# Optimization experiments

Measured on AMD Instinct MI355X. Metric: run time of the kernel, lower is better.

The kernel has to match this reference:

```python
import jax, jax.numpy as jnp
import numpy as np

N_QUBITS = 10
SAMPLE_LENGTH = 2 ** N_QUBITS  # AmplitudeEmbedding requires len(features) == 2**n
NUM_CLASSES = 10
BATCH = 8192
TOTAL_PARAMS = N_QUBITS + 12 * (N_QUBITS // 2) * 2 + N_QUBITS * 3  # 160
C64 = jnp.complex64

H_GATE = (jnp.array([[1, 1], [1, -1]], dtype=C64) * np.float32(1.0 / np.sqrt(2.0)))
CNOT = jnp.array([[1, 0, 0, 0], [0, 1, 0, 0], [0, 0, 0, 1], [0, 0, 1, 0]], dtype=C64)
CZ = jnp.diag(jnp.array([1, 1, 1, -1], dtype=C64))


def rx(t):
    c = jnp.cos(t / 2).astype(C64)
    s = jnp.sin(t / 2).astype(C64)
    return jnp.stack([jnp.stack([c, -1j * s]), jnp.stack([-1j * s, c])])


def ry(t):
    c = jnp.cos(t / 2).astype(C64)
    s = jnp.sin(t / 2).astype(C64)
    return jnp.stack([jnp.stack([c, -s]), jnp.stack([s, c])])


def rz(t):
    e = jnp.exp(-0.5j * t).astype(C64)
    z = jnp.zeros_like(e)
    return jnp.stack([jnp.stack([e, z]), jnp.stack([z, jnp.conj(e)])])


def rot(phi, theta, omega):
    # qml.Rot = RZ(omega) @ RY(theta) @ RZ(phi)
    return rz(omega) @ ry(theta) @ rz(phi)


def apply_gate(psi, U, wires):
    # psi: (B, 2, 2, ..., 2); U: (2**k, 2**k); wires in PennyLane order (wire 0 = MSB = axis 1)
    k = len(wires)
    U = U.reshape((2,) * (2 * k))
    axes = [1 + w for w in wires]
    psi = jnp.tensordot(U, psi, axes=(list(range(k, 2 * k)), axes))
    return jnp.moveaxis(psi, list(range(k)), axes)


def vqc_block(psi, p, i):
    psi = apply_gate(psi, rx(p[0]), [i])
    psi = apply_gate(psi, ry(p[1]), [i + 1])
    psi = apply_gate(psi, ry(p[2]), [i])
    psi = apply_gate(psi, rz(p[3]), [i + 1])
    psi = apply_gate(psi, rz(p[4]), [i])
    psi = apply_gate(psi, rx(p[5]), [i + 1])
    psi = apply_gate(psi, CZ, [i, i + 1])
    psi = apply_gate(psi, rz(p[6]), [i])
    psi = apply_gate(psi, rx(p[7]), [i + 1])
    psi = apply_gate(psi, ry(p[8]), [i])
    psi = apply_gate(psi, rz(p[9]), [i + 1])
    psi = apply_gate(psi, rx(p[10]), [i])
    psi = apply_gate(psi, ry(p[11]), [i + 1])
    psi = apply_gate(psi, CNOT, [i + 1, i])
    return psi


def circuit(x, all_params):
    n = N_QUBITS
    B = x.shape[0]
    # AmplitudeEmbedding with normalize=True
    norm = jnp.linalg.norm(x, axis=1, keepdims=True)
    psi = (x / norm).astype(C64).reshape((B,) + (2,) * n)
    emb = all_params[:n]
    v1 = all_params[n:n + 12 * (n // 2)].reshape(n // 2, 12)
    v2 = all_params[n + 12 * (n // 2):n + 24 * (n // 2)].reshape(n // 2, 12)
    sel = all_params[n + 24 * (n // 2):].reshape(n, 3)
    # embedding layer: H then RY on each wire
    for i in range(n):
        psi = apply_gate(psi, H_GATE, [i])
    for i in range(n):
        psi = apply_gate(psi, ry(emb[i]), [i])
    # two stacks of VQC blocks on even wire pairs
    for i in range(n // 2):
        psi = vqc_block(psi, v1[i], 2 * i)
    for i in range(n // 2):
        psi = vqc_block(psi, v2[i], 2 * i)
    # CNOT ring
    for i in range(n):
        psi = apply_gate(psi, CNOT, [i, (i + 1) % n])
    # StronglyEntanglingLayers, 1 layer: Rot on each wire, then CNOT ring (range=1)
    for i in range(n):
        psi = apply_gate(psi, rot(sel[i, 0], sel[i, 1], sel[i, 2]), [i])
    for i in range(n):
        psi = apply_gate(psi, CNOT, [i, (i + 1) % n])
    # <Z_i> = sum_s |psi_s|^2 * (1 - 2*bit_i(s)), wire 0 = MSB
    probs = (jnp.abs(psi) ** 2).reshape(B, 2 ** n)
    bits = (jnp.arange(2 ** n)[None, :] >> (n - 1 - jnp.arange(n))[:, None]) & 1
    signs = (1 - 2 * bits).astype(jnp.float32)  # (n, 2**n)
    return probs @ signs.T  # (B, n)


def setup_inputs() -> dict:
    key = jax.random.key(0)
    ks = jax.random.split(key, 4)
    x = jax.random.normal(ks[0], (BATCH, SAMPLE_LENGTH), dtype=jnp.float32)
    all_params = jax.random.normal(ks[1], (TOTAL_PARAMS,), dtype=jnp.float32)
    w_in = jax.random.normal(ks[2], (N_QUBITS, SAMPLE_LENGTH), dtype=jnp.float32) * np.float32(1.0 / np.sqrt(SAMPLE_LENGTH))
    b_in = jnp.zeros((N_QUBITS,), dtype=jnp.float32)
    w_fc = jax.random.normal(ks[3], (NUM_CLASSES, N_QUBITS), dtype=jnp.float32) * np.float32(1.0 / np.sqrt(N_QUBITS))
    b_fc = jnp.zeros((NUM_CLASSES,), dtype=jnp.float32)
    return {"x": x, "all_params": all_params, "w_in": w_in, "b_in": b_in, "w_fc": w_fc, "b_fc": b_fc}


def reference(x, all_params, w_in, b_in, w_fc, b_fc):
    x_proj = x @ w_in.T + b_in          # (B, n_qubits)
    q_out = circuit(x, all_params)      # (B, n_qubits)
    q_out = q_out + x_proj              # residual add (dropout is identity at eval)
    return q_out @ w_fc.T + b_fc        # (B, num_classes)
```

## Files before the change

kernel.cpp:

```cpp
#include <hip/hip_runtime.h>

typedef __attribute__((ext_vector_type(2))) float f2;

#define WAIT_LDS asm volatile("s_waitcnt lgkmcnt(0)" ::: "memory")

__device__ __forceinline__ f2 mk(float a, float b){ f2 r; r.x=a; r.y=b; return r; }

template<int CTRL>
__device__ __forceinline__ float dpp_add(float v){
  int t = __builtin_amdgcn_update_dpp(0, __builtin_bit_cast(int, v), CTRL, 0xF, 0xF, true);
  return v + __builtin_bit_cast(float, t);
}
__device__ __forceinline__ float wave_red_bcast(float v){
  v = dpp_add<0x111>(v);
  v = dpp_add<0x112>(v);
  v = dpp_add<0x114>(v);
  v = dpp_add<0x118>(v);
  v = dpp_add<0x142>(v);
  v = dpp_add<0x143>(v);
  return __builtin_bit_cast(float, __builtin_amdgcn_readlane(__builtin_bit_cast(int, v), 63));
}
template<int CTRL>
__device__ __forceinline__ float dpp_qp(float v){
  int t = __builtin_amdgcn_update_dpp(0, __builtin_bit_cast(int, v), CTRL, 0xF, 0xF, true);
  return __builtin_bit_cast(float, t);
}
#define XT(V,o) ((o)==1 ? dpp_qp<0xB1>(V) : (o)==2 ? dpp_qp<0x4E>(V) : __shfl_xor((V),(o)))

__device__ __forceinline__ void cmadS(f2& c, f2 g, f2 b){
  asm("v_pk_fma_f32 %0, %1, %2, %0 op_sel:[0,0,0] op_sel_hi:[0,1,1]\n\t"
      "v_pk_fma_f32 %0, %1, %2, %0 op_sel:[1,1,0] op_sel_hi:[1,0,1] neg_lo:[1,0,0]"
      : "+v"(c) : "s"(g), "v"(b));
}
__device__ __forceinline__ f2 cmulS(f2 g, f2 b){
  f2 d;
  asm("v_pk_mul_f32 %0, %1, %2 op_sel:[0,0] op_sel_hi:[0,1]\n\t"
      "v_pk_fma_f32 %0, %1, %2, %0 op_sel:[1,1,0] op_sel_hi:[1,0,1] neg_lo:[1,0,0]"
      : "=&v"(d) : "s"(g), "v"(b));
  return d;
}
__device__ __forceinline__ void quadS(const f2* __restrict__ G, f2& a0, f2& a1, f2& a2, f2& a3){
  f2 c0,c1,c2,c3;
  c0=cmulS(G[0],a0);  c1=cmulS(G[1],a0);  c2=cmulS(G[2],a0);  c3=cmulS(G[3],a0);
  cmadS(c0,G[4],a1);  cmadS(c1,G[5],a1);  cmadS(c2,G[6],a1);  cmadS(c3,G[7],a1);
  cmadS(c0,G[8],a2);  cmadS(c1,G[9],a2);  cmadS(c2,G[10],a2); cmadS(c3,G[11],a2);
  cmadS(c0,G[12],a3); cmadS(c1,G[13],a3); cmadS(c2,G[14],a3); cmadS(c3,G[15],a3);
  a0=c0; a1=c1; a2=c2; a3=c3;
}

__device__ __forceinline__ float2 cmul(float2 a, float2 b){
  return make_float2(a.x*b.x - a.y*b.y, a.x*b.y + a.y*b.x);
}
__device__ __forceinline__ float2 cmad(float2 acc, float2 a, float2 b){
  acc.x += a.x*b.x - a.y*b.y; acc.y += a.x*b.y + a.y*b.x; return acc;
}

__global__ __launch_bounds__(64) void qm_setup(
    const float* __restrict__ params, const float* __restrict__ w_fc,
    const float* __restrict__ b_in, const float* __restrict__ b_fc,
    float* __restrict__ wsf){
  __shared__ float2 m2[50][4];
  __shared__ float2 h4[10][16];
  const int t = threadIdx.x;

  if (t < 50){
    int typ[5], pix[5], ng;
    if (t < 40){
      int i = t>>3, k = t&7;
      int P1 = 10 + i*12, P2 = 70 + i*12;
      switch(k){
        case 0: ng=5; typ[0]=3;pix[0]=0;     typ[1]=1;pix[1]=2*i;   typ[2]=0;pix[2]=P1+0;
                      typ[3]=1;pix[3]=P1+2;  typ[4]=2;pix[4]=P1+4;  break;
        case 1: ng=5; typ[0]=3;pix[0]=0;     typ[1]=1;pix[1]=2*i+1; typ[2]=1;pix[2]=P1+1;
                      typ[3]=2;pix[3]=P1+3;  typ[4]=0;pix[4]=P1+5;  break;
        case 2: ng=3; typ[0]=2;pix[0]=P1+6;  typ[1]=1;pix[1]=P1+8;  typ[2]=0;pix[2]=P1+10; break;
        case 3: ng=3; typ[0]=0;pix[0]=P1+7;  typ[1]=2;pix[1]=P1+9;  typ[2]=1;pix[2]=P1+11; break;
        case 4: ng=3; typ[0]=0;pix[0]=P2+0;  typ[1]=1;pix[1]=P2+2;  typ[2]=2;pix[2]=P2+4;  break;
        case 5: ng=3; typ[0]=1;pix[0]=P2+1;  typ[1]=2;pix[1]=P2+3;  typ[2]=0;pix[2]=P2+5;  break;
        case 6: ng=3; typ[0]=2;pix[0]=P2+6;  typ[1]=1;pix[1]=P2+8;  typ[2]=0;pix[2]=P2+10; break;
        default:ng=3; typ[0]=0;pix[0]=P2+7;  typ[1]=2;pix[1]=P2+9;  typ[2]=1;pix[2]=P2+11; break;
      }
    } else {
      int S = 130 + (t-40)*3;
      ng=3; typ[0]=2;pix[0]=S+0; typ[1]=1;pix[1]=S+1; typ[2]=2;pix[2]=S+2;
    }
    float2 M[4] = {{1.f,0.f},{0.f,0.f},{0.f,0.f},{1.f,0.f}};
    #pragma clang loop unroll(disable)
    for (int g=0; g<ng; ++g){
      float2 R[4];
      if (typ[g]==3){
        const float r_=0.70710678118654752f;
        R[0]={r_,0.f}; R[1]={r_,0.f}; R[2]={r_,0.f}; R[3]={-r_,0.f};
      } else {
        float th = params[pix[g]]*0.5f;
        float c = cosf(th), s = sinf(th);
        if (typ[g]==0){ R[0]={c,0.f}; R[1]={0.f,-s}; R[2]={0.f,-s}; R[3]={c,0.f}; }
        else if (typ[g]==1){ R[0]={c,0.f}; R[1]={-s,0.f}; R[2]={s,0.f}; R[3]={c,0.f}; }
        else { R[0]={c,-s}; R[1]={0.f,0.f}; R[2]={0.f,0.f}; R[3]={c,s}; }
      }
      float2 T0=cmad(cmul(R[0],M[0]), R[1], M[2]);
      float2 T1=cmad(cmul(R[0],M[1]), R[1], M[3]);
      float2 T2=cmad(cmul(R[2],M[0]), R[3], M[2]);
      float2 T3=cmad(cmul(R[2],M[1]), R[3], M[3]);
      M[0]=T0; M[1]=T1; M[2]=T2; M[3]=T3;
    }
    m2[t][0]=M[0]; m2[t][1]=M[1]; m2[t][2]=M[2]; m2[t][3]=M[3];
  }
  __syncthreads();
  if (t < 10){
    int i = t>>1, L = t&1;
    const float2* A1 = m2[i*8 + L*4 + 0];
    const float2* B1 = m2[i*8 + L*4 + 1];
    const float2* A2 = m2[i*8 + L*4 + 2];
    const float2* B2 = m2[i*8 + L*4 + 3];
    float2 K1[16], K2[16];
    #pragma clang loop unroll(disable)
    for (int r=0;r<4;r++)
      #pragma clang loop unroll(disable)
      for (int c=0;c<4;c++){
        K1[r*4+c] = cmul(A1[(r>>1)*2+(c>>1)], B1[(r&1)*2+(c&1)]);
        K2[r*4+c] = cmul(A2[(r>>1)*2+(c>>1)], B2[(r&1)*2+(c&1)]);
      }
    #pragma clang loop unroll(disable)
    for (int c=0;c<4;c++){ K1[12+c].x=-K1[12+c].x; K1[12+c].y=-K1[12+c].y; }
    #pragma clang loop unroll(disable)
    for (int r=0;r<4;r++){
      int rr = (r==1)?3:(r==3)?1:r;
      #pragma clang loop unroll(disable)
      for (int c=0;c<4;c++){
        float2 v = cmul(K2[r*4+0], K1[0+c]);
        v = cmad(v, K2[r*4+1], K1[4+c]);
        v = cmad(v, K2[r*4+2], K1[8+c]);
        v = cmad(v, K2[r*4+3], K1[12+c]);
        h4[t][rr*4+c] = v;
      }
    }
  }
  __syncthreads();
  if (t < 5){
    const float2* Ga = h4[t*2+1];
    const float2* Gb = h4[t*2+0];
    float2* dst = (float2*)wsf + t*16;
    #pragma clang loop unroll(disable)
    for (int r=0;r<4;r++)
      #pragma clang loop unroll(disable)
      for (int c=0;c<4;c++){
        float2 v = cmul(Ga[r*4+0], Gb[0+c]);
        v = cmad(v, Ga[r*4+1], Gb[4+c]);
        v = cmad(v, Ga[r*4+2], Gb[8+c]);
        v = cmad(v, Ga[r*4+3], Gb[12+c]);
        dst[c*4+r] = v;
      }
  } else if (t < 10){
    int i = t-5;
    const float2* Ra = m2[40 + 2*i];
    const float2* Rb = m2[40 + 2*i + 1];
    float2* dst = (float2*)wsf + 80 + i*16;
    #pragma clang loop unroll(disable)
    for (int r=0;r<4;r++)
      #pragma clang loop unroll(disable)
      for (int c=0;c<4;c++)
        dst[c*4+r] = cmul(Ra[(r>>1)*2+(c>>1)], Rb[(r&1)*2+(c&1)]);
  } else if (t < 20){
    int c = t-10;
    float s = b_fc[c];
    #pragma clang loop unroll(disable)
    for (int q=0;q<10;q++) s += w_fc[c*10+q]*b_in[q];
    wsf[320+c] = s;
  }
}

#define SGN_IP(V, o) { float t_=XT(V,o); float d_=V-t_; V = (l&(o))?-d_:d_; }
#define PLAIN_IP(V, o) { V += XT(V,o); }
#define SPLIT(Vp, Vs, V, o) { float t_=XT(V,o); Vp = V+t_; float d_=V-t_; Vs=(l&(o))?-d_:d_; }

__global__ __launch_bounds__(128,5) void qm_sim(
    const float* __restrict__ x, const float* __restrict__ w_in,
    const float* __restrict__ w_fc, const float* __restrict__ wsf,
    float* __restrict__ out)
{
  __shared__ __align__(16) f2 psi[2048];
  const int t = threadIdx.x;
  const int l = t & 63, wid = t >> 6;
  const int sample = (blockIdx.x<<1) + wid;
  char* PB = (char*)(psi + (wid<<10));
  const float* xr = x + ((size_t)sample<<10);
  const f2* G = (const f2*)wsf;

  float4 xv0 = *(const float4*)(xr + (l<<4));
  float4 xv1 = *(const float4*)(xr + (l<<4) + 4);
  float4 xv2 = *(const float4*)(xr + (l<<4) + 8);
  float4 xv3 = *(const float4*)(xr + (l<<4) + 12);
  f2 xc[8];
  xc[0]=mk(xv0.x,xv0.y); xc[1]=mk(xv0.z,xv0.w); xc[2]=mk(xv1.x,xv1.y); xc[3]=mk(xv1.z,xv1.w);
  xc[4]=mk(xv2.x,xv2.y); xc[5]=mk(xv2.z,xv2.w); xc[6]=mk(xv3.x,xv3.y); xc[7]=mk(xv3.z,xv3.w);
  float xp[10];
  #pragma unroll
  for (int q=0;q<10;q++){
    const float4* wr = (const float4*)(w_in + (q<<10) + (l<<4));
    float4 w0=wr[0], w1=wr[1], w2=wr[2], w3=wr[3];
    f2 a;
    a  = xc[0]*mk(w0.x,w0.y);
    a += xc[1]*mk(w0.z,w0.w);
    a += xc[2]*mk(w1.x,w1.y);
    a += xc[3]*mk(w1.z,w1.w);
    a += xc[4]*mk(w2.x,w2.y);
    a += xc[5]*mk(w2.z,w2.w);
    a += xc[6]*mk(w3.x,w3.y);
    a += xc[7]*mk(w3.z,w3.w);
    xp[q] = a.x + a.y;
  }
  f2 nn = xc[0]*xc[0]; nn += xc[1]*xc[1]; nn += xc[2]*xc[2]; nn += xc[3]*xc[3];
  nn += xc[4]*xc[4]; nn += xc[5]*xc[5]; nn += xc[6]*xc[6]; nn += xc[7]*xc[7];
  float xs[16];
  #pragma unroll
  for (int k=0;k<16;k++) xs[k] = xr[(k<<6)|l];
  float rn = rsqrtf(wave_red_bcast(nn.x + nn.y));

  f2 A[16];
  #pragma unroll
  for (int k=0;k<16;k++) A[k] = mk(xs[k]*rn, 0.f);
  #pragma unroll
  for (int j=0;j<4;j++) quadS(G+ 0, A[j], A[4+j], A[8+j], A[12+j]);
  #pragma unroll
  for (int i=0;i<4;i++) quadS(G+16, A[4*i], A[4*i+1], A[4*i+2], A[4*i+3]);
  const int Lb = (l ^ (l>>4)) << 3;
  #pragma unroll
  for (int k=0;k<16;k++){
    const int ck = (((k<<6) ^ ((k&3)<<2)) << 3);
    *(f2*)(PB + (Lb ^ ck)) = A[k];
  }
  WAIT_LDS;

  const int L2 = ((((l>>2)<<6)) ^ (l&3) ^ (l&0xC)) << 3;
  #pragma unroll
  for (int k=0;k<16;k++){
    const int ck = (((k<<2) ^ (k>>2)) << 3);
    A[k] = *(const f2*)(PB + (L2 ^ ck));
  }
  #pragma unroll
  for (int j=0;j<4;j++) quadS(G+32, A[j], A[4+j], A[8+j], A[12+j]);
  #pragma unroll
  for (int i=0;i<4;i++) quadS(G+48, A[4*i], A[4*i+1], A[4*i+2], A[4*i+3]);
  #pragma unroll
  for (int k=0;k<16;k++){
    const int ck = (((k<<2) ^ (k>>2)) << 3);
    *(f2*)(PB + (L2 ^ ck)) = A[k];
  }
  WAIT_LDS;

  {
    const int L3 = (((l<<4) ^ (l<<3)) ^ ((l ^ (l>>1)) & 15)) << 3;
    const int IOFF[4] = {0, 0x6, 0xC, 0xA};
    #pragma unroll
    for (int k=0;k<16;k++){
      const int ck = ((IOFF[k>>2] ^ (k&3)) << 3);
      A[k] = *(const f2*)(PB + (L3 ^ ck));
    }
    quadS(G+64, A[0], A[1], A[2], A[3]);
    quadS(G+64, A[6], A[7], A[4], A[5]);
    quadS(G+64, A[8], A[9], A[10], A[11]);
    quadS(G+64, A[14], A[15], A[12], A[13]);
    #pragma unroll
    for (int j=0;j<4;j++) quadS(G+128, A[j], A[4+j], A[8+j], A[12+j]);
    const int L3w = ((l<<4) ^ (l&15)) << 3;
    const int PJ[4] = {0, 0x201, 0x203, 0x002};
    #pragma unroll
    for (int k=0;k<16;k++){
      const int ck = (((k & 0xC) ^ PJ[k&3]) << 3);
      *(f2*)(PB + (L3w ^ ck)) = A[k];
    }
  }
  WAIT_LDS;

  #pragma unroll
  for (int k=0;k<16;k++){
    const int ck = (((k<<6) ^ ((k&3)<<2)) << 3);
    A[k] = *(const f2*)(PB + (Lb ^ ck));
  }
  #pragma unroll
  for (int j=0;j<4;j++) quadS(G+80, A[j], A[4+j], A[8+j], A[12+j]);
  #pragma unroll
  for (int i=0;i<4;i++) quadS(G+96, A[4*i], A[4*i+1], A[4*i+2], A[4*i+3]);
  #pragma unroll
  for (int k=0;k<16;k++){
    const int ck = (((k<<6) ^ ((k&3)<<2)) << 3);
    *(f2*)(PB + (Lb ^ ck)) = A[k];
  }
  WAIT_LDS;

  const int L5 = ((((l>>2)<<6)) ^ ((l&3)<<2) ^ (l&0xC)) << 3;
  #pragma unroll
  for (int k=0;k<16;k++){
    const int ck = ((((k>>2)<<4) ^ (k>>2) ^ (k&3)) << 3);
    A[k] = *(const f2*)(PB + (L5 ^ ck));
  }
  #pragma unroll
  for (int j=0;j<4;j++) quadS(G+112, A[j], A[4+j], A[8+j], A[12+j]);
  #pragma unroll
  for (int i=0;i<4;i++) quadS(G+144, A[4*i], A[4*i+1], A[4*i+2], A[4*i+3]);

  float p[16];
  #pragma unroll
  for (int k=0;k<16;k++){ f2 sq = A[k]*A[k]; p[k] = sq.x + sq.y; }
  float sg[4], eg[4], fg[4];
  #pragma unroll
  for (int g=0; g<4; ++g){
    float a_=p[4*g]+p[4*g+1], b_=p[4*g+2]+p[4*g+3];
    float c_=p[4*g]-p[4*g+1], d_=p[4*g+2]-p[4*g+3];
    sg[g]=a_+b_; eg[g]=a_-b_; fg[g]=c_-d_;
  }
  float s01=sg[0]+sg[1], s23=sg[2]+sg[3];
  float d01=sg[0]-sg[1], d23=sg[2]-sg[3];
  float S  = s01+s23;
  float W8 = s01-s23;
  float WC = d01-d23;
  float WE = (eg[0]-eg[1])-(eg[2]-eg[3]);
  float WF = (fg[0]-fg[1])-(fg[2]-fg[3]);
  float WCp, WCs, WCpp, WCps, WCss, Sp, Ss, Spp, Sps, q0;
  PLAIN_IP(S,1); PLAIN_IP(W8,1); SPLIT(WCp, WCs, WC, 1); SGN_IP(WE,1); SGN_IP(WF,1);
  PLAIN_IP(S,2); PLAIN_IP(W8,2); SPLIT(WCpp, WCps, WCp, 2); SGN_IP(WCs,2); SGN_IP(WE,2); SGN_IP(WF,2);
  WCss = WCs;
  SPLIT(Sp, Ss, S, 4); SGN_IP(W8,4); SGN_IP(WCpp,4); SGN_IP(WCps,4); SGN_IP(WCss,4); SGN_IP(WE,4); SGN_IP(WF,4);
  SPLIT(Spp, Sps, Sp, 8); SGN_IP(Ss,8); SGN_IP(W8,8); SGN_IP(WCpp,8); SGN_IP(WCps,8); SGN_IP(WCss,8); SGN_IP(WE,8); SGN_IP(WF,8);
  SGN_IP(Spp,16); SGN_IP(Sps,16); SGN_IP(Ss,16); SGN_IP(W8,16); SGN_IP(WCpp,16);
  SGN_IP(WCps,16); SGN_IP(WCss,16); SGN_IP(WE,16); SGN_IP(WF,16);
  SGN_IP(Spp,32); SGN_IP(Sps,32); SGN_IP(Ss,32); SGN_IP(W8,32); SGN_IP(WCpp,32);
  SGN_IP(WCps,32); SGN_IP(WCss,32); SGN_IP(WE,32);
  { float t_=__shfl_xor(WF,32); q0 = WF+t_; float d_=WF-t_; WF=(l&32)?-d_:d_; }

  float xqs[10];
  #pragma unroll
  for (int q=0;q<10;q++) xqs[q] = wave_red_bcast(xp[q]);

  if (l < 10){
    float W[10] = {q0, Spp, Sps, Ss, W8, WCpp, WCps, WCss, WE, WF};
    float o = wsf[320+l];
    const float* wf = w_fc + l*10;
    #pragma unroll
    for (int q=0;q<10;q++) o += wf[q] * (W[q] + xqs[q]);
    out[(size_t)sample*10 + l] = o;
  }
}

extern "C" void kernel_launch(void* const* d_in, const int* in_sizes, int n_in,
                              void* d_out, int out_size, void* d_ws, size_t ws_size,
                              hipStream_t stream) {
  const float* x      = (const float*)d_in[0];
  const float* params = (const float*)d_in[1];
  const float* w_in   = (const float*)d_in[2];
  const float* b_in   = (const float*)d_in[3];
  const float* w_fc   = (const float*)d_in[4];
  const float* b_fc   = (const float*)d_in[5];
  float* out = (float*)d_out;

  float* wsf = (float*)d_ws;

  int batch = in_sizes[0] >> 10;

  qm_setup<<<dim3(1), dim3(64), 0, stream>>>(params, w_fc, b_in, b_fc, wsf);
  qm_sim<<<dim3(batch>>1), dim3(128), 0, stream>>>(x, w_in, w_fc, wsf, out);
}
```

Baseline: 64.17 us.

## Process two samples per wavefront to interleave independent gate chains

Each wave now simulates two samples with interleaved register state, so the LDS transposes and gate arithmetic of two independent chains can hide each other's latency. The w_in loads in the projection are shared across both samples through cache. The shared buffer doubles, launch bounds drop to 2 waves-per-EU hints, and the grid halves. Register pressure roughly doubles, which lowers occupancy and may cause spills.

```diff
diff --git a/kernel.cpp b/kernel.cpp
--- a/kernel.cpp
+++ b/kernel.cpp
@@ -170,23 +170,38 @@
   }
 }
 
-#define SGN_IP(V, o) { float t_=XT(V,o); float d_=V-t_; V = (l&(o))?-d_:d_; }
-#define PLAIN_IP(V, o) { V += XT(V,o); }
-#define SPLIT(Vp, Vs, V, o) { float t_=XT(V,o); Vp = V+t_; float d_=V-t_; Vs=(l&(o))?-d_:d_; }
-
-__global__ __launch_bounds__(128,5) void qm_sim(
-    const float* __restrict__ x, const float* __restrict__ w_in,
-    const float* __restrict__ w_fc, const float* __restrict__ wsf,
-    float* __restrict__ out)
-{
-  __shared__ __align__(16) f2 psi[2048];
-  const int t = threadIdx.x;
-  const int l = t & 63, wid = t >> 6;
-  const int sample = (blockIdx.x<<1) + wid;
-  char* PB = (char*)(psi + (wid<<10));
-  const float* xr = x + ((size_t)sample<<10);
-  const f2* G = (const f2*)wsf;
-
+template<int F> __device__ __forceinline__ int ckf(int k){
+  if constexpr (F==1) return (((k<<6) ^ ((k&3)<<2)) << 3);
+  else if constexpr (F==2) return (((k<<2) ^ (k>>2)) << 3);
+  else if constexpr (F==3){ constexpr int IOFF[4]={0,0x6,0xC,0xA}; return ((IOFF[k>>2] ^ (k&3)) << 3); }
+  else if constexpr (F==4){ constexpr int PJ[4]={0,0x201,0x203,0x002}; return (((k&0xC) ^ PJ[k&3]) << 3); }
+  else return ((((k>>2)<<4) ^ (k>>2) ^ (k&3)) << 3);
+}
+template<int F> __device__ __forceinline__ void stA(char* PB, int L, const f2* A){
+  #pragma unroll
+  for (int k=0;k<16;k++) *(f2*)(PB + (L ^ ckf<F>(k))) = A[k];
+}
+template<int F> __device__ __forceinline__ void ldA(char* PB, int L, f2* A){
+  #pragma unroll
+  for (int k=0;k<16;k++) A[k] = *(const f2*)(PB + (L ^ ckf<F>(k)));
+}
+__device__ __forceinline__ void gij(const f2* Gi, const f2* Gj, f2* A){
+  #pragma unroll
+  for (int j=0;j<4;j++) quadS(Gi, A[j], A[4+j], A[8+j], A[12+j]);
+  #pragma unroll
+  for (int i=0;i<4;i++) quadS(Gj, A[4*i], A[4*i+1], A[4*i+2], A[4*i+3]);
+}
+__device__ __forceinline__ void g3(const f2* G10, const f2* Gr32, f2* A){
+  quadS(G10, A[0], A[1], A[2], A[3]);
+  quadS(G10, A[6], A[7], A[4], A[5]);
+  quadS(G10, A[8], A[9], A[10], A[11]);
+  quadS(G10, A[14], A[15], A[12], A[13]);
+  #pragma unroll
+  for (int j=0;j<4;j++) quadS(Gr32, A[j], A[4+j], A[8+j], A[12+j]);
+}
+
+__device__ __forceinline__ void gemv(const float* __restrict__ xr, const float* __restrict__ w_in,
+                                     int l, float* xp, float* xs, float& n2raw){
   float4 xv0 = *(const float4*)(xr + (l<<4));
   float4 xv1 = *(const float4*)(xr + (l<<4) + 4);
   float4 xv2 = *(const float4*)(xr + (l<<4) + 8);
@@ -194,7 +209,6 @@
   f2 xc[8];
   xc[0]=mk(xv0.x,xv0.y); xc[1]=mk(xv0.z,xv0.w); xc[2]=mk(xv1.x,xv1.y); xc[3]=mk(xv1.z,xv1.w);
   xc[4]=mk(xv2.x,xv2.y); xc[5]=mk(xv2.z,xv2.w); xc[6]=mk(xv3.x,xv3.y); xc[7]=mk(xv3.z,xv3.w);
-  float xp[10];
   #pragma unroll
   for (int q=0;q<10;q++){
     const float4* wr = (const float4*)(w_in + (q<<10) + (l<<4));
@@ -212,94 +226,16 @@
   }
   f2 nn = xc[0]*xc[0]; nn += xc[1]*xc[1]; nn += xc[2]*xc[2]; nn += xc[3]*xc[3];
   nn += xc[4]*xc[4]; nn += xc[5]*xc[5]; nn += xc[6]*xc[6]; nn += xc[7]*xc[7];
-  float xs[16];
+  n2raw = nn.x + nn.y;
   #pragma unroll
   for (int k=0;k<16;k++) xs[k] = xr[(k<<6)|l];
-  float rn = rsqrtf(wave_red_bcast(nn.x + nn.y));
-
-  f2 A[16];
-  #pragma unroll
-  for (int k=0;k<16;k++) A[k] = mk(xs[k]*rn, 0.f);
-  #pragma unroll
-  for (int j=0;j<4;j++) quadS(G+ 0, A[j], A[4+j], A[8+j], A[12+j]);
-  #pragma unroll
-  for (int i=0;i<4;i++) quadS(G+16, A[4*i], A[4*i+1], A[4*i+2], A[4*i+3]);
-  const int Lb = (l ^ (l>>4)) << 3;
-  #pragma unroll
-  for (int k=0;k<16;k++){
-    const int ck = (((k<<6) ^ ((k&3)<<2)) << 3);
-    *(f2*)(PB + (Lb ^ ck)) = A[k];
-  }
-  WAIT_LDS;
-
-  const int L2 = ((((l>>2)<<6)) ^ (l&3) ^ (l&0xC)) << 3;
-  #pragma unroll
-  for (int k=0;k<16;k++){
-    const int ck = (((k<<2) ^ (k>>2)) << 3);
-    A[k] = *(const f2*)(PB + (L2 ^ ck));
-  }
-  #pragma unroll
-  for (int j=0;j<4;j++) quadS(G+32, A[j], A[4+j], A[8+j], A[12+j]);
-  #pragma unroll
-  for (int i=0;i<4;i++) quadS(G+48, A[4*i], A[4*i+1], A[4*i+2], A[4*i+3]);
-  #pragma unroll
-  for (int k=0;k<16;k++){
-    const int ck = (((k<<2) ^ (k>>2)) << 3);
-    *(f2*)(PB + (L2 ^ ck)) = A[k];
-  }
-  WAIT_LDS;
-
-  {
-    const int L3 = (((l<<4) ^ (l<<3)) ^ ((l ^ (l>>1)) & 15)) << 3;
-    const int IOFF[4] = {0, 0x6, 0xC, 0xA};
-    #pragma unroll
-    for (int k=0;k<16;k++){
-      const int ck = ((IOFF[k>>2] ^ (k&3)) << 3);
-      A[k] = *(const f2*)(PB + (L3 ^ ck));
-    }
-    quadS(G+64, A[0], A[1], A[2], A[3]);
-    quadS(G+64, A[6], A[7], A[4], A[5]);
-    quadS(G+64, A[8], A[9], A[10], A[11]);
-    quadS(G+64, A[14], A[15], A[12], A[13]);
-    #pragma unroll
-    for (int j=0;j<4;j++) quadS(G+128, A[j], A[4+j], A[8+j], A[12+j]);
-    const int L3w = ((l<<4) ^ (l&15)) << 3;
-    const int PJ[4] = {0, 0x201, 0x203, 0x002};
-    #pragma unroll
-    for (int k=0;k<16;k++){
-      const int ck = (((k & 0xC) ^ PJ[k&3]) << 3);
-      *(f2*)(PB + (L3w ^ ck)) = A[k];
-    }
-  }
-  WAIT_LDS;
-
-  #pragma unroll
-  for (int k=0;k<16;k++){
-    const int ck = (((k<<6) ^ ((k&3)<<2)) << 3);
-    A[k] = *(const f2*)(PB + (Lb ^ ck));
-  }
-  #pragma unroll
-  for (int j=0;j<4;j++) quadS(G+80, A[j], A[4+j], A[8+j], A[12+j]);
-  #pragma unroll
-  for (int i=0;i<4;i++) quadS(G+96, A[4*i], A[4*i+1], A[4*i+2], A[4*i+3]);
-  #pragma unroll
-  for (int k=0;k<16;k++){
-    const int ck = (((k<<6) ^ ((k&3)<<2)) << 3);
-    *(f2*)(PB + (Lb ^ ck)) = A[k];
-  }
-  WAIT_LDS;
-
-  const int L5 = ((((l>>2)<<6)) ^ ((l&3)<<2) ^ (l&0xC)) << 3;
-  #pragma unroll
-  for (int k=0;k<16;k++){
-    const int ck = ((((k>>2)<<4) ^ (k>>2) ^ (k&3)) << 3);
-    A[k] = *(const f2*)(PB + (L5 ^ ck));
-  }
-  #pragma unroll
-  for (int j=0;j<4;j++) quadS(G+112, A[j], A[4+j], A[8+j], A[12+j]);
-  #pragma unroll
-  for (int i=0;i<4;i++) quadS(G+144, A[4*i], A[4*i+1], A[4*i+2], A[4*i+3]);
-
+}
+
+#define SGN_IP(V, o) { float t_=XT(V,o); float d_=V-t_; V = (l&(o))?-d_:d_; }
+#define PLAIN_IP(V, o) { V += XT(V,o); }
+#define SPLIT(Vp, Vs, V, o) { float t_=XT(V,o); Vp = V+t_; float d_=V-t_; Vs=(l&(o))?-d_:d_; }
+
+__device__ __forceinline__ void walsh(const f2* A, int l, float* W){
   float p[16];
   #pragma unroll
   for (int k=0;k<16;k++){ f2 sq = A[k]*A[k]; p[k] = sq.x + sq.y; }
@@ -328,18 +264,78 @@
   SGN_IP(Spp,32); SGN_IP(Sps,32); SGN_IP(Ss,32); SGN_IP(W8,32); SGN_IP(WCpp,32);
   SGN_IP(WCps,32); SGN_IP(WCss,32); SGN_IP(WE,32);
   { float t_=__shfl_xor(WF,32); q0 = WF+t_; float d_=WF-t_; WF=(l&32)?-d_:d_; }
-
-  float xqs[10];
-  #pragma unroll
-  for (int q=0;q<10;q++) xqs[q] = wave_red_bcast(xp[q]);
+  W[0]=q0; W[1]=Spp; W[2]=Sps; W[3]=Ss; W[4]=W8;
+  W[5]=WCpp; W[6]=WCps; W[7]=WCss; W[8]=WE; W[9]=WF;
+}
+
+__global__ __launch_bounds__(128,2) void qm_sim(
+    const float* __restrict__ x, const float* __restrict__ w_in,
+    const float* __restrict__ w_fc, const float* __restrict__ wsf,
+    float* __restrict__ out)
+{
+  __shared__ __align__(16) f2 psi[4096];
+  const int t = threadIdx.x;
+  const int l = t & 63, wid = t >> 6;
+  const int s0 = (blockIdx.x<<2) + (wid<<1), s1 = s0 + 1;
+  char* PB0 = (char*)(psi + (wid<<11));
+  char* PB1 = PB0 + 8192;
+  const float* xr0 = x + ((size_t)s0<<10);
+  const float* xr1 = x + ((size_t)s1<<10);
+  const f2* G = (const f2*)wsf;
+
+  float xp0[10], xp1[10], xs0[16], xs1[16], n2a, n2b;
+  gemv(xr0, w_in, l, xp0, xs0, n2a);
+  gemv(xr1, w_in, l, xp1, xs1, n2b);
+  float rn0 = rsqrtf(wave_red_bcast(n2a));
+  float rn1 = rsqrtf(wave_red_bcast(n2b));
+
+  const int Lb  = (l ^ (l>>4)) << 3;
+  const int L2  = ((((l>>2)<<6)) ^ (l&3) ^ (l&0xC)) << 3;
+  const int L3  = (((l<<4) ^ (l<<3)) ^ ((l ^ (l>>1)) & 15)) << 3;
+  const int L3w = ((l<<4) ^ (l&15)) << 3;
+  const int L5  = ((((l>>2)<<6)) ^ ((l&3)<<2) ^ (l&0xC)) << 3;
+
+  f2 A0[16], A1[16];
+  #pragma unroll
+  for (int k=0;k<16;k++){ A0[k] = mk(xs0[k]*rn0, 0.f); A1[k] = mk(xs1[k]*rn1, 0.f); }
+  gij(G+ 0, G+16, A0);  gij(G+ 0, G+16, A1);
+  stA<1>(PB0, Lb, A0);  stA<1>(PB1, Lb, A1);
+  WAIT_LDS;
+  ldA<2>(PB0, L2, A0);  ldA<2>(PB1, L2, A1);
+  gij(G+32, G+48, A0);  gij(G+32, G+48, A1);
+  stA<2>(PB0, L2, A0);  stA<2>(PB1, L2, A1);
+  WAIT_LDS;
+  ldA<3>(PB0, L3, A0);  ldA<3>(PB1, L3, A1);
+  g3(G+64, G+128, A0);  g3(G+64, G+128, A1);
+  stA<4>(PB0, L3w, A0); stA<4>(PB1, L3w, A1);
+  WAIT_LDS;
+  ldA<1>(PB0, Lb, A0);  ldA<1>(PB1, Lb, A1);
+  gij(G+80, G+96, A0);  gij(G+80, G+96, A1);
+  stA<1>(PB0, Lb, A0);  stA<1>(PB1, Lb, A1);
+  WAIT_LDS;
+  ldA<5>(PB0, L5, A0);  ldA<5>(PB1, L5, A1);
+  gij(G+112, G+144, A0); gij(G+112, G+144, A1);
+
+  float W0[10], W1[10];
+  walsh(A0, l, W0);
+  walsh(A1, l, W1);
+  float xq0[10], xq1[10];
+  #pragma unroll
+  for (int q=0;q<10;q++){ xq0[q] = wave_red_bcast(xp0[q]); xq1[q] = wave_red_bcast(xp1[q]); }
 
   if (l < 10){
-    float W[10] = {q0, Spp, Sps, Ss, W8, WCpp, WCps, WCss, WE, WF};
-    float o = wsf[320+l];
-    const float* wf = w_fc + l*10;
+    float cb = wsf[320+l];
+    float wf[10];
     #pragma unroll
-    for (int q=0;q<10;q++) o += wf[q] * (W[q] + xqs[q]);
-    out[(size_t)sample*10 + l] = o;
+    for (int q=0;q<10;q++) wf[q] = w_fc[l*10+q];
+    float o0 = cb, o1 = cb;
+    #pragma unroll
+    for (int q=0;q<10;q++){
+      o0 += wf[q] * (W0[q] + xq0[q]);
+      o1 += wf[q] * (W1[q] + xq1[q]);
+    }
+    out[(size_t)s0*10 + l] = o0;
+    out[(size_t)s1*10 + l] = o1;
   }
 }
 
@@ -359,5 +355,5 @@
   int batch = in_sizes[0] >> 10;
 
   qm_setup<<<dim3(1), dim3(64), 0, stream>>>(params, w_fc, b_in, b_fc, wsf);
-  qm_sim<<<dim3(batch>>1), dim3(128), 0, stream>>>(x, w_in, w_fc, wsf, out);
-}
+  qm_sim<<<dim3(batch>>2), dim3(128), 0, stream>>>(x, w_in, w_fc, wsf, out);
+}
```

After: 65.30 us. About the same (+1.8%).

## Halve per-wave LDS scratch via staged two-phase state exchanges, four waves per block

Applied to the files above, without the earlier changes.

Each wave's LDS state buffer shrinks from 1024 to 512 complex entries. The transposes between gate stages now run in two half-wave or half-state phases, with extra register staging (T[8]) and more waitcnt points. Blocks grow to 256 threads covering four samples, and the x-projection reductions are folded into the first loop. The goal is more resident waves per CU, since LDS use per sample was limiting occupancy. The cost is more LDS round trips, divergent branches and higher register pressure.

```diff
diff --git a/kernel.cpp b/kernel.cpp
--- a/kernel.cpp
+++ b/kernel.cpp
@@ -170,136 +170,33 @@
   }
 }
 
+constexpr int CK1(int k){ return ((((k<<6) ^ ((k&3)<<2)) << 3) & 0xFFF); }
+constexpr int CK2(int k){ return (((k<<2) ^ (k>>2)) << 3); }
+constexpr int CK3(int k){ constexpr int IOFF[4]={0,0x6,0xC,0xA}; return ((IOFF[k>>2] ^ (k&3)) << 3); }
+constexpr int CK4(int k){ constexpr int PJ[4]={0,0x201,0x203,0x002};
+                          return ((((k&0xC) ^ PJ[k&3]) << 3) & 0xFFF); }
+constexpr int CK5(int k){ return ((((k>>2)<<4) ^ (k>>2) ^ (k&3)) << 3); }
+
+__device__ __forceinline__ void gij(const f2* Gi, const f2* Gj, f2* A){
+  #pragma unroll
+  for (int j=0;j<4;j++) quadS(Gi, A[j], A[4+j], A[8+j], A[12+j]);
+  #pragma unroll
+  for (int i=0;i<4;i++) quadS(Gj, A[4*i], A[4*i+1], A[4*i+2], A[4*i+3]);
+}
+__device__ __forceinline__ void g3(const f2* G10, const f2* Gr32, f2* A){
+  quadS(G10, A[0], A[1], A[2], A[3]);
+  quadS(G10, A[6], A[7], A[4], A[5]);
+  quadS(G10, A[8], A[9], A[10], A[11]);
+  quadS(G10, A[14], A[15], A[12], A[13]);
+  #pragma unroll
+  for (int j=0;j<4;j++) quadS(Gr32, A[j], A[4+j], A[8+j], A[12+j]);
+}
+
 #define SGN_IP(V, o) { float t_=XT(V,o); float d_=V-t_; V = (l&(o))?-d_:d_; }
 #define PLAIN_IP(V, o) { V += XT(V,o); }
 #define SPLIT(Vp, Vs, V, o) { float t_=XT(V,o); Vp = V+t_; float d_=V-t_; Vs=(l&(o))?-d_:d_; }
 
-__global__ __launch_bounds__(128,5) void qm_sim(
-    const float* __restrict__ x, const float* __restrict__ w_in,
-    const float* __restrict__ w_fc, const float* __restrict__ wsf,
-    float* __restrict__ out)
-{
-  __shared__ __align__(16) f2 psi[2048];
-  const int t = threadIdx.x;
-  const int l = t & 63, wid = t >> 6;
-  const int sample = (blockIdx.x<<1) + wid;
-  char* PB = (char*)(psi + (wid<<10));
-  const float* xr = x + ((size_t)sample<<10);
-  const f2* G = (const f2*)wsf;
-
-  float4 xv0 = *(const float4*)(xr + (l<<4));
-  float4 xv1 = *(const float4*)(xr + (l<<4) + 4);
-  float4 xv2 = *(const float4*)(xr + (l<<4) + 8);
-  float4 xv3 = *(const float4*)(xr + (l<<4) + 12);
-  f2 xc[8];
-  xc[0]=mk(xv0.x,xv0.y); xc[1]=mk(xv0.z,xv0.w); xc[2]=mk(xv1.x,xv1.y); xc[3]=mk(xv1.z,xv1.w);
-  xc[4]=mk(xv2.x,xv2.y); xc[5]=mk(xv2.z,xv2.w); xc[6]=mk(xv3.x,xv3.y); xc[7]=mk(xv3.z,xv3.w);
-  float xp[10];
-  #pragma unroll
-  for (int q=0;q<10;q++){
-    const float4* wr = (const float4*)(w_in + (q<<10) + (l<<4));
-    float4 w0=wr[0], w1=wr[1], w2=wr[2], w3=wr[3];
-    f2 a;
-    a  = xc[0]*mk(w0.x,w0.y);
-    a += xc[1]*mk(w0.z,w0.w);
-    a += xc[2]*mk(w1.x,w1.y);
-    a += xc[3]*mk(w1.z,w1.w);
-    a += xc[4]*mk(w2.x,w2.y);
-    a += xc[5]*mk(w2.z,w2.w);
-    a += xc[6]*mk(w3.x,w3.y);
-    a += xc[7]*mk(w3.z,w3.w);
-    xp[q] = a.x + a.y;
-  }
-  f2 nn = xc[0]*xc[0]; nn += xc[1]*xc[1]; nn += xc[2]*xc[2]; nn += xc[3]*xc[3];
-  nn += xc[4]*xc[4]; nn += xc[5]*xc[5]; nn += xc[6]*xc[6]; nn += xc[7]*xc[7];
-  float xs[16];
-  #pragma unroll
-  for (int k=0;k<16;k++) xs[k] = xr[(k<<6)|l];
-  float rn = rsqrtf(wave_red_bcast(nn.x + nn.y));
-
-  f2 A[16];
-  #pragma unroll
-  for (int k=0;k<16;k++) A[k] = mk(xs[k]*rn, 0.f);
-  #pragma unroll
-  for (int j=0;j<4;j++) quadS(G+ 0, A[j], A[4+j], A[8+j], A[12+j]);
-  #pragma unroll
-  for (int i=0;i<4;i++) quadS(G+16, A[4*i], A[4*i+1], A[4*i+2], A[4*i+3]);
-  const int Lb = (l ^ (l>>4)) << 3;
-  #pragma unroll
-  for (int k=0;k<16;k++){
-    const int ck = (((k<<6) ^ ((k&3)<<2)) << 3);
-    *(f2*)(PB + (Lb ^ ck)) = A[k];
-  }
-  WAIT_LDS;
-
-  const int L2 = ((((l>>2)<<6)) ^ (l&3) ^ (l&0xC)) << 3;
-  #pragma unroll
-  for (int k=0;k<16;k++){
-    const int ck = (((k<<2) ^ (k>>2)) << 3);
-    A[k] = *(const f2*)(PB + (L2 ^ ck));
-  }
-  #pragma unroll
-  for (int j=0;j<4;j++) quadS(G+32, A[j], A[4+j], A[8+j], A[12+j]);
-  #pragma unroll
-  for (int i=0;i<4;i++) quadS(G+48, A[4*i], A[4*i+1], A[4*i+2], A[4*i+3]);
-  #pragma unroll
-  for (int k=0;k<16;k++){
-    const int ck = (((k<<2) ^ (k>>2)) << 3);
-    *(f2*)(PB + (L2 ^ ck)) = A[k];
-  }
-  WAIT_LDS;
-
-  {
-    const int L3 = (((l<<4) ^ (l<<3)) ^ ((l ^ (l>>1)) & 15)) << 3;
-    const int IOFF[4] = {0, 0x6, 0xC, 0xA};
-    #pragma unroll
-    for (int k=0;k<16;k++){
-      const int ck = ((IOFF[k>>2] ^ (k&3)) << 3);
-      A[k] = *(const f2*)(PB + (L3 ^ ck));
-    }
-    quadS(G+64, A[0], A[1], A[2], A[3]);
-    quadS(G+64, A[6], A[7], A[4], A[5]);
-    quadS(G+64, A[8], A[9], A[10], A[11]);
-    quadS(G+64, A[14], A[15], A[12], A[13]);
-    #pragma unroll
-    for (int j=0;j<4;j++) quadS(G+128, A[j], A[4+j], A[8+j], A[12+j]);
-    const int L3w = ((l<<4) ^ (l&15)) << 3;
-    const int PJ[4] = {0, 0x201, 0x203, 0x002};
-    #pragma unroll
-    for (int k=0;k<16;k++){
-      const int ck = (((k & 0xC) ^ PJ[k&3]) << 3);
-      *(f2*)(PB + (L3w ^ ck)) = A[k];
-    }
-  }
-  WAIT_LDS;
-
-  #pragma unroll
-  for (int k=0;k<16;k++){
-    const int ck = (((k<<6) ^ ((k&3)<<2)) << 3);
-    A[k] = *(const f2*)(PB + (Lb ^ ck));
-  }
-  #pragma unroll
-  for (int j=0;j<4;j++) quadS(G+80, A[j], A[4+j], A[8+j], A[12+j]);
-  #pragma unroll
-  for (int i=0;i<4;i++) quadS(G+96, A[4*i], A[4*i+1], A[4*i+2], A[4*i+3]);
-  #pragma unroll
-  for (int k=0;k<16;k++){
-    const int ck = (((k<<6) ^ ((k&3)<<2)) << 3);
-    *(f2*)(PB + (Lb ^ ck)) = A[k];
-  }
-  WAIT_LDS;
-
-  const int L5 = ((((l>>2)<<6)) ^ ((l&3)<<2) ^ (l&0xC)) << 3;
-  #pragma unroll
-  for (int k=0;k<16;k++){
-    const int ck = ((((k>>2)<<4) ^ (k>>2) ^ (k&3)) << 3);
-    A[k] = *(const f2*)(PB + (L5 ^ ck));
-  }
-  #pragma unroll
-  for (int j=0;j<4;j++) quadS(G+112, A[j], A[4+j], A[8+j], A[12+j]);
-  #pragma unroll
-  for (int i=0;i<4;i++) quadS(G+144, A[4*i], A[4*i+1], A[4*i+2], A[4*i+3]);
-
+__device__ __forceinline__ void walsh(const f2* A, int l, float* W){
   float p[16];
   #pragma unroll
   for (int k=0;k<16;k++){ f2 sq = A[k]*A[k]; p[k] = sq.x + sq.y; }
@@ -328,17 +225,179 @@
   SGN_IP(Spp,32); SGN_IP(Sps,32); SGN_IP(Ss,32); SGN_IP(W8,32); SGN_IP(WCpp,32);
   SGN_IP(WCps,32); SGN_IP(WCss,32); SGN_IP(WE,32);
   { float t_=__shfl_xor(WF,32); q0 = WF+t_; float d_=WF-t_; WF=(l&32)?-d_:d_; }
-
-  float xqs[10];
-  #pragma unroll
-  for (int q=0;q<10;q++) xqs[q] = wave_red_bcast(xp[q]);
+  W[0]=q0; W[1]=Spp; W[2]=Sps; W[3]=Ss; W[4]=W8;
+  W[5]=WCpp; W[6]=WCps; W[7]=WCss; W[8]=WE; W[9]=WF;
+}
+
+__global__ __launch_bounds__(256,6) void qm_sim(
+    const float* __restrict__ x, const float* __restrict__ w_in,
+    const float* __restrict__ w_fc, const float* __restrict__ wsf,
+    float* __restrict__ out)
+{
+  __shared__ __align__(16) f2 psi[2048];
+  const int t = threadIdx.x;
+  const int l = t & 63, wid = t >> 6;
+  const int sample = (blockIdx.x<<2) + wid;
+  char* PB = (char*)(psi + (wid<<9));
+  const float* xr = x + ((size_t)sample<<10);
+  const f2* G = (const f2*)wsf;
+
+  float xq[10], n2;
+  {
+    float4 xv0 = *(const float4*)(xr + (l<<4));
+    float4 xv1 = *(const float4*)(xr + (l<<4) + 4);
+    float4 xv2 = *(const float4*)(xr + (l<<4) + 8);
+    float4 xv3 = *(const float4*)(xr + (l<<4) + 12);
+    f2 xc[8];
+    xc[0]=mk(xv0.x,xv0.y); xc[1]=mk(xv0.z,xv0.w); xc[2]=mk(xv1.x,xv1.y); xc[3]=mk(xv1.z,xv1.w);
+    xc[4]=mk(xv2.x,xv2.y); xc[5]=mk(xv2.z,xv2.w); xc[6]=mk(xv3.x,xv3.y); xc[7]=mk(xv3.z,xv3.w);
+    #pragma unroll
+    for (int q=0;q<10;q++){
+      const float4* wr = (const float4*)(w_in + (q<<10) + (l<<4));
+      float4 w0=wr[0], w1=wr[1], w2=wr[2], w3=wr[3];
+      f2 a;
+      a  = xc[0]*mk(w0.x,w0.y);
+      a += xc[1]*mk(w0.z,w0.w);
+      a += xc[2]*mk(w1.x,w1.y);
+      a += xc[3]*mk(w1.z,w1.w);
+      a += xc[4]*mk(w2.x,w2.y);
+      a += xc[5]*mk(w2.z,w2.w);
+      a += xc[6]*mk(w3.x,w3.y);
+      a += xc[7]*mk(w3.z,w3.w);
+      xq[q] = wave_red_bcast(a.x + a.y);
+    }
+    f2 nn = xc[0]*xc[0]; nn += xc[1]*xc[1]; nn += xc[2]*xc[2]; nn += xc[3]*xc[3];
+    nn += xc[4]*xc[4]; nn += xc[5]*xc[5]; nn += xc[6]*xc[6]; nn += xc[7]*xc[7];
+    n2 = nn.x + nn.y;
+  }
+  float xs[16];
+  #pragma unroll
+  for (int k=0;k<16;k++) xs[k] = xr[(k<<6)|l];
+  float rn = rsqrtf(wave_red_bcast(n2));
+
+  const int Lb  = (l ^ (l>>4)) << 3;
+  const int L2m = (((((l>>2)<<6)) ^ (l&3) ^ (l&0xC)) << 3) & 0xFFF;
+  const int L3m = ((((l<<4) ^ (l<<3)) ^ ((l ^ (l>>1)) & 15)) << 3) & 0xFFF;
+  const int L3wm= (((l<<4) ^ (l&15)) << 3) & 0xFFF;
+  const int L5m = (((((l>>2)<<6)) ^ ((l&3)<<2) ^ (l&0xC)) << 3) & 0xFFF;
+  const bool hi = (l & 32) != 0;
+
+  f2 A[16], T[8];
+
+  #pragma unroll
+  for (int k=0;k<16;k++) A[k] = mk(xs[k]*rn, 0.f);
+  gij(G+ 0, G+16, A);
+
+  #pragma unroll
+  for (int k=0;k<8;k++) *(f2*)(PB + (Lb ^ CK1(k))) = A[k];
+  WAIT_LDS;
+  if (!hi){
+    #pragma unroll
+    for (int k=0;k<8;k++) A[k] = *(const f2*)(PB + (L2m ^ CK2(k)));
+    #pragma unroll
+    for (int k=0;k<8;k++) T[k] = *(const f2*)(PB + (L2m ^ CK2(k+8)));
+  }
+  WAIT_LDS;
+  #pragma unroll
+  for (int k=8;k<16;k++) *(f2*)(PB + (Lb ^ CK1(k))) = A[k];
+  WAIT_LDS;
+  if (hi){
+    #pragma unroll
+    for (int k=0;k<16;k++) A[k] = *(const f2*)(PB + (L2m ^ CK2(k)));
+  } else {
+    #pragma unroll
+    for (int k=0;k<8;k++) A[8+k] = T[k];
+  }
+  WAIT_LDS;
+
+  gij(G+32, G+48, A);
+
+  if (!hi){
+    #pragma unroll
+    for (int k=0;k<16;k++) *(f2*)(PB + (L2m ^ CK2(k))) = A[k];
+  }
+  WAIT_LDS;
+  if (!hi){
+    #pragma unroll
+    for (int k=0;k<16;k++) A[k] = *(const f2*)(PB + (L3m ^ CK3(k)));
+  }
+  WAIT_LDS;
+  if (hi){
+    #pragma unroll
+    for (int k=0;k<16;k++) *(f2*)(PB + (L2m ^ CK2(k))) = A[k];
+  }
+  WAIT_LDS;
+  if (hi){
+    #pragma unroll
+    for (int k=0;k<16;k++) A[k] = *(const f2*)(PB + (L3m ^ CK3(k)));
+  }
+  WAIT_LDS;
+
+  g3(G+64, G+128, A);
+
+  {
+    const int K03[8] = {0,3,4,7,8,11,12,15};
+    const int K12[8] = {1,2,5,6,9,10,13,14};
+    if (!hi){
+      #pragma unroll
+      for (int m=0;m<8;m++){ int k=K03[m]; *(f2*)(PB + (L3wm ^ CK4(k))) = A[k]; }
+    } else {
+      #pragma unroll
+      for (int m=0;m<8;m++){ int k=K12[m]; *(f2*)(PB + (L3wm ^ CK4(k))) = A[k]; }
+    }
+    WAIT_LDS;
+    #pragma unroll
+    for (int k=0;k<8;k++) T[k] = *(const f2*)(PB + (Lb ^ CK1(k)));
+    WAIT_LDS;
+    if (hi){
+      #pragma unroll
+      for (int m=0;m<8;m++){ int k=K03[m]; *(f2*)(PB + (L3wm ^ CK4(k))) = A[k]; }
+    } else {
+      #pragma unroll
+      for (int m=0;m<8;m++){ int k=K12[m]; *(f2*)(PB + (L3wm ^ CK4(k))) = A[k]; }
+    }
+    WAIT_LDS;
+    #pragma unroll
+    for (int k=8;k<16;k++) A[k] = *(const f2*)(PB + (Lb ^ CK1(k)));
+    #pragma unroll
+    for (int k=0;k<8;k++) A[k] = T[k];
+    WAIT_LDS;
+  }
+
+  gij(G+80, G+96, A);
+
+  #pragma unroll
+  for (int k=0;k<8;k++) *(f2*)(PB + (Lb ^ CK1(k))) = A[k];
+  WAIT_LDS;
+  if (!hi){
+    #pragma unroll
+    for (int k=0;k<8;k++) A[k] = *(const f2*)(PB + (L5m ^ CK5(k)));
+    #pragma unroll
+    for (int k=0;k<8;k++) T[k] = *(const f2*)(PB + (L5m ^ CK5(k+8)));
+  }
+  WAIT_LDS;
+  #pragma unroll
+  for (int k=8;k<16;k++) *(f2*)(PB + (Lb ^ CK1(k))) = A[k];
+  WAIT_LDS;
+  if (hi){
+    #pragma unroll
+    for (int k=0;k<16;k++) A[k] = *(const f2*)(PB + (L5m ^ CK5(k)));
+  } else {
+    #pragma unroll
+    for (int k=0;k<8;k++) A[8+k] = T[k];
+  }
+  WAIT_LDS;
+
+  gij(G+112, G+144, A);
+
+  float W[10];
+  walsh(A, l, W);
 
   if (l < 10){
-    float W[10] = {q0, Spp, Sps, Ss, W8, WCpp, WCps, WCss, WE, WF};
     float o = wsf[320+l];
     const float* wf = w_fc + l*10;
     #pragma unroll
-    for (int q=0;q<10;q++) o += wf[q] * (W[q] + xqs[q]);
+    for (int q=0;q<10;q++) o += wf[q] * (W[q] + xq[q]);
     out[(size_t)sample*10 + l] = o;
   }
 }
@@ -359,5 +418,5 @@
   int batch = in_sizes[0] >> 10;
 
   qm_setup<<<dim3(1), dim3(64), 0, stream>>>(params, w_fc, b_in, b_fc, wsf);
-  qm_sim<<<dim3(batch>>1), dim3(128), 0, stream>>>(x, w_in, w_fc, wsf, out);
-}
+  qm_sim<<<dim3(batch>>2), dim3(256), 0, stream>>>(x, w_in, w_fc, wsf, out);
+}
```

New measurement: 58.21 us. 1.1x faster.
